# Kernel optimization log

Hardware: AMD Instinct MI355X
Metric: run time of the kernel (lower is better)

The kernel has to match this reference:

```python
import jax, jax.numpy as jnp
import numpy as np

N_NODES = 100000
N_EDGES = 1200000
D = 64


def gcn_conv(x, src, dst, ew, W, b, n):
    # add self-loops with weight 1 (PyG GCNConv default)
    loops = jnp.arange(n)
    s = jnp.concatenate([src, loops])
    d = jnp.concatenate([dst, loops])
    w = jnp.concatenate([ew, jnp.ones((n,), ew.dtype)])
    deg = jax.ops.segment_sum(w, d, num_segments=n)           # [n]
    dis = jnp.where(deg > 0, jax.lax.rsqrt(deg), 0.0)
    norm = dis[s] * w * dis[d]                                # [E+n]
    h = x @ W                                                 # [n, out]
    msg = norm[:, None] * h[s]                                # gather
    out = jax.ops.segment_sum(msg, d, num_segments=n)         # scatter
    return out + b


def setup_inputs() -> dict:
    key = jax.random.key(0)
    ks = jax.random.split(key, 7)
    x = jax.random.normal(ks[0], (N_NODES, D), dtype=jnp.float32)
    edge_index = jax.random.randint(ks[1], (2, N_EDGES), 0, N_NODES, dtype=jnp.int64)
    edge_weight = jax.random.uniform(ks[2], (N_EDGES,), dtype=jnp.float32)
    W1 = jax.random.normal(ks[3], (D, D), dtype=jnp.float32) * (1.0 / np.sqrt(D))
    b1 = jnp.zeros((D,), dtype=jnp.float32)
    W2 = jax.random.normal(ks[4], (D, D), dtype=jnp.float32) * (1.0 / np.sqrt(D))
    b2 = jnp.zeros((D,), dtype=jnp.float32)
    return {"x": x, "edge_index": edge_index, "edge_weight": edge_weight,
            "W1": W1, "b1": b1, "W2": W2, "b2": b2}


def reference(x, edge_index, edge_weight, W1, b1, W2, b2):
    n = x.shape[0]
    src, dst = edge_index[0], edge_index[1]
    x1 = jax.nn.relu(gcn_conv(x, src, dst, edge_weight, W1, b1, n))
    x2 = jax.nn.relu(gcn_conv(x1, src, dst, edge_weight, W2, b2, n))
    return (x1 + x2) * 0.5
```

## Files before the change

### kernel.cpp

```cpp
#include <hip/hip_runtime.h>

#define NN 100000
#define NE 1200000
#define DD 64
#define NBUCK 196
#define BCAP 7168
#define TILE 4096
#define NB1 293
#define NB_G 1563
#define FIX25 33554432.0f
#define FIX25_INV (1.0f/33554432.0f)

typedef short bf16x8 __attribute__((ext_vector_type(8)));
typedef float f32x4  __attribute__((ext_vector_type(4)));

static __device__ __forceinline__ unsigned short f2bf(float f) {
    unsigned int u = __float_as_uint(f);
    unsigned int r = (u + 0x7fffu + ((u >> 16) & 1u)) >> 16;
    return (unsigned short)r;
}
static __device__ __forceinline__ float bf2f(unsigned short s) {
    return __uint_as_float(((unsigned int)s) << 16);
}


__global__ __launch_bounds__(256) void prep(
    int* __restrict__ cursor,
    const float* __restrict__ W1, const float* __restrict__ W2,
    unsigned short* __restrict__ Wt1, unsigned short* __restrict__ Wt2)
{
    if (blockIdx.x == 0) {
        if (threadIdx.x < NBUCK) cursor[threadIdx.x] = 0;
        return;
    }
    const float* W = (blockIdx.x == 1) ? W1 : W2;
    unsigned short* Wt = (blockIdx.x == 1) ? Wt1 : Wt2;
    int t = threadIdx.x;
    int col = t >> 2, k0 = (t & 3) * 16;
    #pragma unroll
    for (int i = 0; i < 16; ++i)
        Wt[col * 64 + k0 + i] = f2bf(W[(k0 + i) * 64 + col]);
}


static __device__ __forceinline__ void gemm_body(
    const float* __restrict__ x, const unsigned short* __restrict__ Wt,
    unsigned short* __restrict__ h16, int r0, int t,
    unsigned short* Xs, unsigned short* Ws)
{
    {
        int col = t >> 2, seg = (t & 3) * 16;
        const uint4* p = (const uint4*)(Wt + col * 64 + seg);
        uint4 a0 = p[0], a1 = p[1];
        *(uint4*)&Ws[col * 72 + seg]     = a0;
        *(uint4*)&Ws[col * 72 + seg + 8] = a1;
    }
    {
        int row = t >> 2, seg = (t & 3) * 16;
        int gr = r0 + row;
        float4 v0 = {0,0,0,0}, v1 = v0, v2 = v0, v3 = v0;
        if (gr < NN) {
            const float4* p = (const float4*)(x + (size_t)gr * DD + seg);
            v0 = p[0]; v1 = p[1]; v2 = p[2]; v3 = p[3];
        }
        ushort4 h0 = { f2bf(v0.x), f2bf(v0.y), f2bf(v0.z), f2bf(v0.w) };
        ushort4 h1 = { f2bf(v1.x), f2bf(v1.y), f2bf(v1.z), f2bf(v1.w) };
        ushort4 h2 = { f2bf(v2.x), f2bf(v2.y), f2bf(v2.z), f2bf(v2.w) };
        ushort4 h3 = { f2bf(v3.x), f2bf(v3.y), f2bf(v3.z), f2bf(v3.w) };
        *(ushort4*)&Xs[row * 72 + seg]      = h0;
        *(ushort4*)&Xs[row * 72 + seg + 4]  = h1;
        *(ushort4*)&Xs[row * 72 + seg + 8]  = h2;
        *(ushort4*)&Xs[row * 72 + seg + 12] = h3;
    }
    __syncthreads();

    const int wv = t >> 6;
    const int ln = t & 63;
    const int m  = ln & 15;
    const int q  = ln >> 4;
    const int arow = wv * 16 + m;

    bf16x8 a0 = *(const bf16x8*)&Xs[arow * 72 + q * 8];
    bf16x8 a1 = *(const bf16x8*)&Xs[arow * 72 + 32 + q * 8];

    f32x4 acc[4];
    #pragma unroll
    for (int c = 0; c < 4; ++c) {
        bf16x8 b0 = *(const bf16x8*)&Ws[(c * 16 + m) * 72 + q * 8];
        bf16x8 b1 = *(const bf16x8*)&Ws[(c * 16 + m) * 72 + 32 + q * 8];
        f32x4 z = {0.f, 0.f, 0.f, 0.f};
        z = __builtin_amdgcn_mfma_f32_16x16x32_bf16(a0, b0, z, 0, 0, 0);
        z = __builtin_amdgcn_mfma_f32_16x16x32_bf16(a1, b1, z, 0, 0, 0);
        acc[c] = z;
    }

    #pragma unroll
    for (int r = 0; r < 4; ++r) {
        int grow = r0 + wv * 16 + q * 4 + r;
        if (grow < NN) {
            #pragma unroll
            for (int c = 0; c < 4; ++c)
                h16[(size_t)grow * DD + c * 16 + m] = f2bf(acc[c][r]);
        }
    }
}


__global__ __launch_bounds__(256) void pass1_gemm(
    const int* __restrict__ src, const int* __restrict__ dst,
    const float* __restrict__ ew, int* __restrict__ cursor,
    unsigned long long* __restrict__ stage,
    const float* __restrict__ x, const unsigned short* __restrict__ Wt1,
    unsigned short* __restrict__ h16)
{
    __shared__ unsigned short Xs[64 * 72];
    __shared__ unsigned short Ws[64 * 72];
    __shared__ int cnt[NBUCK];
    __shared__ int resv[NBUCK];

    const int t = threadIdx.x;

    if (blockIdx.x >= NB1) {
        gemm_body(x, Wt1, h16, (blockIdx.x - NB1) * 64, t, Xs, Ws);
        return;
    }

    const int base = blockIdx.x * TILE;
    if (t < NBUCK) cnt[t] = 0;
    __syncthreads();

    #pragma unroll
    for (int k = 0; k < TILE / 256; ++k) {
        int e = base + k * 256 + t;
        if (e < NE) atomicAdd(&cnt[dst[e] >> 9], 1);
    }
    __syncthreads();
    if (t < NBUCK) {
        int c = cnt[t];
        resv[t] = c ? atomicAdd(&cursor[t], c) : 0;
        cnt[t] = 0;
    }
    __syncthreads();
    #pragma unroll
    for (int k = 0; k < TILE / 256; ++k) {
        int e = base + k * 256 + t;
        if (e < NE) {
            int d = dst[e];
            int b = d >> 9;
            int r = atomicAdd(&cnt[b], 1);
            int pos = resv[b] + r;
            if (pos < BCAP) {
                unsigned int meta = ((unsigned int)(d & 511) << 17) |
                                    (unsigned int)src[e];
                stage[(size_t)b * BCAP + pos] =
                    ((unsigned long long)meta << 32) | __float_as_uint(ew[e]);
            }
        }
    }
}


__global__ __launch_bounds__(512) void pass2(
    const unsigned long long* __restrict__ stage, const int* __restrict__ cursor,
    unsigned int* __restrict__ csr, unsigned int* __restrict__ rowdeg,
    float* __restrict__ dis)
{
    __shared__ unsigned long long sb[BCAP];
    __shared__ int cnt[512];
    __shared__ unsigned sum[512];
    __shared__ int lptr[512];

    const int b = blockIdx.x;
    const int t = threadIdx.x;
    const int n0 = b << 9;
    const int cntb = min(cursor[b], BCAP);

    cnt[t] = 0; sum[t] = 0;
    __syncthreads();

    for (int k = t; k < cntb; k += 512) {
        unsigned long long E = stage[(size_t)b * BCAP + k];
        unsigned int meta = (unsigned int)(E >> 32);
        int dl = meta >> 17;
        float w = __uint_as_float((unsigned int)E);
        int r = atomicAdd(&cnt[dl], 1);
        atomicAdd(&sum[dl], (unsigned)(w * FIX25));
        unsigned int meta2 = ((unsigned int)dl << 23) |
                             ((unsigned int)min(r, 63) << 17) |
                             (meta & 0x1ffffu);
        sb[k] = ((unsigned long long)meta2 << 32) |
                ((r < 64) ? (unsigned long long)f2bf(w) : 0xffffffffull);
    }
    __syncthreads();

    int v = cnt[t];
    __syncthreads();
    for (int off = 1; off < 512; off <<= 1) {
        int add = (t >= off) ? cnt[t - off] : 0;
        __syncthreads();
        cnt[t] += add;
        __syncthreads();
    }
    lptr[t] = cnt[t] - v;

    int node = n0 + t;
    if (node < NN) {
        float deg = 1.0f + (float)sum[t] * FIX25_INV;
        dis[node] = rsqrtf(deg);
        rowdeg[node] = ((unsigned)(b * BCAP + (cnt[t] - v)) << 6) |
                       (unsigned)min(v, 63);
    }
    __syncthreads();

    for (int k = t; k < cntb; k += 512) {
        unsigned long long E = sb[k];
        if ((unsigned int)E == 0xffffffffu) continue;
        unsigned int meta2 = (unsigned int)(E >> 32);
        int dl = meta2 >> 23;
        int r  = (meta2 >> 17) & 63;
        unsigned int s = meta2 & 0x1ffffu;
        csr[b * BCAP + lptr[dl] + r] =
            (s << 15) | ((unsigned int)E & 0x7fffu);
    }
}


__global__ __launch_bounds__(256) void bake(
    unsigned int* __restrict__ csr, const int* __restrict__ cursor,
    const float* __restrict__ dis)
{
    const int b  = blockIdx.x / 7;
    const int k0 = (blockIdx.x % 7) * 1024;
    const int cntb = min(cursor[b], BCAP);
    const int kend = min(k0 + 1024, cntb);
    for (int k = k0 + threadIdx.x; k < kend; k += 256) {
        unsigned int e = csr[b * BCAP + k];
        unsigned int s = e >> 15;
        float nm = dis[s] * bf2f((unsigned short)(e & 0x7fffu));
        csr[b * BCAP + k] = (e & 0xffff8000u) | (f2bf(nm) & 0x7fffu);
    }
}


template <bool FINAL>
__global__ __launch_bounds__(256) void gather(
    const unsigned short* __restrict__ h16, const float* __restrict__ bias,
    const float* __restrict__ dis, const unsigned int* __restrict__ rowdeg,
    const unsigned int* __restrict__ csr,
    const float* __restrict__ prev, float* __restrict__ out)
{
    const int node = __builtin_amdgcn_readfirstlane(
        (blockIdx.x * blockDim.x + threadIdx.x) >> 6);
    const int lane = threadIdx.x & 63;
    if (node >= NN) return;

    const unsigned int rd = rowdeg[node];
    const int deg = rd & 63;
    const float di = dis[node];

    float a0 = fmaf(di * di, bf2f(h16[node * DD + lane]), bias[lane]);
    float a1 = 0.f, a2 = 0.f, a3 = 0.f;

    const unsigned int* seg = csr + (rd >> 6);
    int j = 0;
    for (; j + 3 < deg; j += 4) {
        unsigned int e0 = seg[j],     e1 = seg[j + 1];
        unsigned int e2 = seg[j + 2], e3 = seg[j + 3];
        float n0 = bf2f((unsigned short)(e0 & 0x7fffu)) * di;
        float n1 = bf2f((unsigned short)(e1 & 0x7fffu)) * di;
        float n2 = bf2f((unsigned short)(e2 & 0x7fffu)) * di;
        float n3 = bf2f((unsigned short)(e3 & 0x7fffu)) * di;
        a0 = fmaf(n0, bf2f(h16[(e0 >> 15) * DD + lane]), a0);
        a1 = fmaf(n1, bf2f(h16[(e1 >> 15) * DD + lane]), a1);
        a2 = fmaf(n2, bf2f(h16[(e2 >> 15) * DD + lane]), a2);
        a3 = fmaf(n3, bf2f(h16[(e3 >> 15) * DD + lane]), a3);
    }
    for (; j < deg; ++j) {
        unsigned int e = seg[j];
        a0 = fmaf(bf2f((unsigned short)(e & 0x7fffu)) * di,
                  bf2f(h16[(e >> 15) * DD + lane]), a0);
    }

    float v = fmaxf((a0 + a1) + (a2 + a3), 0.f);
    int idx = node * DD + lane;
    if (FINAL) out[idx] = 0.5f * (prev[idx] + v);
    else       out[idx] = v;
}

__global__ __launch_bounds__(256) void gemm_mfma(
    const float* __restrict__ x, const unsigned short* __restrict__ Wt,
    unsigned short* __restrict__ h16)
{
    __shared__ unsigned short Xs[64 * 72];
    __shared__ unsigned short Ws[64 * 72];
    gemm_body(x, Wt, h16, blockIdx.x * 64, threadIdx.x, Xs, Ws);
}


extern "C" void kernel_launch(void* const* d_in, const int* in_sizes, int n_in,
                              void* d_out, int out_size, void* d_ws, size_t ws_size,
                              hipStream_t stream) {
    const float* x   = (const float*)d_in[0];
    const int*   ei  = (const int*)d_in[1];
    const float* ewt = (const float*)d_in[2];
    const float* W1  = (const float*)d_in[3];
    const float* b1  = (const float*)d_in[4];
    const float* W2  = (const float*)d_in[5];
    const float* b2  = (const float*)d_in[6];
    float* out = (float*)d_out;

    const int* srcv = ei;
    const int* dstv = ei + NE;

    float* wsf = (float*)d_ws;
    int* cursor = (int*)wsf;
    unsigned short* Wt1 = (unsigned short*)(wsf + 256);
    unsigned short* Wt2 = Wt1 + 4096;
    float* dis = wsf + 4352;
    unsigned int* rowdeg = (unsigned int*)(wsf + 104448);
    unsigned long long* stage = (unsigned long long*)(wsf + 204544);
    unsigned int* csr = (unsigned int*)(wsf + 204544 + 2 * NBUCK * BCAP);
    unsigned short* h16 = (unsigned short*)(csr + NBUCK * BCAP);

    const int GB = (NN * 64) / 256;

    prep<<<3, 256, 0, stream>>>(cursor, W1, W2, Wt1, Wt2);
    pass1_gemm<<<NB1 + NB_G, 256, 0, stream>>>(srcv, dstv, ewt, cursor, stage,
                                               x, Wt1, h16);
    pass2<<<NBUCK, 512, 0, stream>>>(stage, cursor, csr, rowdeg, dis);
    bake<<<NBUCK * 7, 256, 0, stream>>>(csr, cursor, dis);

    gather<false><<<GB, 256, 0, stream>>>(h16, b1, dis, rowdeg, csr, nullptr, out);
    gemm_mfma<<<NB_G, 256, 0, stream>>>(out, Wt2, h16);
    gather<true><<<GB, 256, 0, stream>>>(h16, b2, dis, rowdeg, csr, out, out);
}
```

Before: 229.0 us.

## Drop prep and bake kernels, re-read stage in pass2, shuffle edges in gather

The prep kernel is replaced by a memset plus W transposition and bf16 conversion done inside each GEMM block, and the bake kernel is removed. Source normalisation dis[s] is now applied in gather, where each lane loads one CSR entry and the edges are broadcast with wave shuffles. pass2 no longer stages edges in a large LDS buffer and instead re-reads the global stage array in a second pass. The pass1 tile is doubled so fewer blocks do the bucketing. Together these cut kernel launches and LDS use, at the cost of extra global reads in pass2 and a per-edge dis gather in each gather kernel.

```diff
diff --git a/kernel.cpp b/kernel.cpp
--- a/kernel.cpp
+++ b/kernel.cpp
@@ -5,8 +5,8 @@
 #define DD 64
 #define NBUCK 196
 #define BCAP 7168
-#define TILE 4096
-#define NB1 293
+#define TILE 8192
+#define NB1 147
 #define NB_G 1563
 #define FIX25 33554432.0f
 #define FIX25_INV (1.0f/33554432.0f)
@@ -24,36 +24,16 @@
 }
 
 
-__global__ __launch_bounds__(256) void prep(
-    int* __restrict__ cursor,
-    const float* __restrict__ W1, const float* __restrict__ W2,
-    unsigned short* __restrict__ Wt1, unsigned short* __restrict__ Wt2)
-{
-    if (blockIdx.x == 0) {
-        if (threadIdx.x < NBUCK) cursor[threadIdx.x] = 0;
-        return;
-    }
-    const float* W = (blockIdx.x == 1) ? W1 : W2;
-    unsigned short* Wt = (blockIdx.x == 1) ? Wt1 : Wt2;
-    int t = threadIdx.x;
-    int col = t >> 2, k0 = (t & 3) * 16;
-    #pragma unroll
-    for (int i = 0; i < 16; ++i)
-        Wt[col * 64 + k0 + i] = f2bf(W[(k0 + i) * 64 + col]);
-}
-
-
 static __device__ __forceinline__ void gemm_body(
-    const float* __restrict__ x, const unsigned short* __restrict__ Wt,
+    const float* __restrict__ x, const float* __restrict__ W,
     unsigned short* __restrict__ h16, int r0, int t,
     unsigned short* Xs, unsigned short* Ws)
 {
     {
-        int col = t >> 2, seg = (t & 3) * 16;
-        const uint4* p = (const uint4*)(Wt + col * 64 + seg);
-        uint4 a0 = p[0], a1 = p[1];
-        *(uint4*)&Ws[col * 72 + seg]     = a0;
-        *(uint4*)&Ws[col * 72 + seg + 8] = a1;
+        int col = t >> 2, k0 = (t & 3) * 16;
+        #pragma unroll
+        for (int i = 0; i < 16; ++i)
+            Ws[col * 72 + k0 + i] = f2bf(W[(k0 + i) * 64 + col]);
     }
     {
         int row = t >> 2, seg = (t & 3) * 16;
@@ -110,7 +90,7 @@
     const int* __restrict__ src, const int* __restrict__ dst,
     const float* __restrict__ ew, int* __restrict__ cursor,
     unsigned long long* __restrict__ stage,
-    const float* __restrict__ x, const unsigned short* __restrict__ Wt1,
+    const float* __restrict__ x, const float* __restrict__ W1,
     unsigned short* __restrict__ h16)
 {
     __shared__ unsigned short Xs[64 * 72];
@@ -121,7 +101,7 @@
     const int t = threadIdx.x;
 
     if (blockIdx.x >= NB1) {
-        gemm_body(x, Wt1, h16, (blockIdx.x - NB1) * 64, t, Xs, Ws);
+        gemm_body(x, W1, h16, (blockIdx.x - NB1) * 64, t, Xs, Ws);
         return;
     }
 
@@ -129,7 +109,7 @@
     if (t < NBUCK) cnt[t] = 0;
     __syncthreads();
 
-    #pragma unroll
+    #pragma unroll 8
     for (int k = 0; k < TILE / 256; ++k) {
         int e = base + k * 256 + t;
         if (e < NE) atomicAdd(&cnt[dst[e] >> 9], 1);
@@ -141,7 +121,7 @@
         cnt[t] = 0;
     }
     __syncthreads();
-    #pragma unroll
+    #pragma unroll 8
     for (int k = 0; k < TILE / 256; ++k) {
         int e = base + k * 256 + t;
         if (e < NE) {
@@ -165,9 +145,9 @@
     unsigned int* __restrict__ csr, unsigned int* __restrict__ rowdeg,
     float* __restrict__ dis)
 {
-    __shared__ unsigned long long sb[BCAP];
     __shared__ int cnt[512];
     __shared__ unsigned sum[512];
+    __shared__ int scn[512];
     __shared__ int lptr[512];
 
     const int b = blockIdx.x;
@@ -176,6 +156,36 @@
     const int cntb = min(cursor[b], BCAP);
 
     cnt[t] = 0; sum[t] = 0;
+    __syncthreads();
+
+    for (int k = t; k < cntb; k += 512) {
+        unsigned long long E = stage[(size_t)b * BCAP + k];
+        int dl = (int)(E >> 49);
+        float w = __uint_as_float((unsigned int)E);
+        atomicAdd(&cnt[dl], 1);
+        atomicAdd(&sum[dl], (unsigned)(w * FIX25));
+    }
+    __syncthreads();
+
+    int v = cnt[t];
+    scn[t] = v;
+    __syncthreads();
+    for (int off = 1; off < 512; off <<= 1) {
+        int add = (t >= off) ? scn[t - off] : 0;
+        __syncthreads();
+        scn[t] += add;
+        __syncthreads();
+    }
+    lptr[t] = scn[t] - v;
+    cnt[t] = 0;
+
+    int node = n0 + t;
+    if (node < NN) {
+        float deg = 1.0f + (float)sum[t] * FIX25_INV;
+        dis[node] = rsqrtf(deg);
+        rowdeg[node] = ((unsigned)(b * BCAP + lptr[t]) << 6) |
+                       (unsigned)min(v, 63);
+    }
     __syncthreads();
 
     for (int k = t; k < cntb; k += 512) {
@@ -184,60 +194,9 @@
         int dl = meta >> 17;
         float w = __uint_as_float((unsigned int)E);
         int r = atomicAdd(&cnt[dl], 1);
-        atomicAdd(&sum[dl], (unsigned)(w * FIX25));
-        unsigned int meta2 = ((unsigned int)dl << 23) |
-                             ((unsigned int)min(r, 63) << 17) |
-                             (meta & 0x1ffffu);
-        sb[k] = ((unsigned long long)meta2 << 32) |
-                ((r < 64) ? (unsigned long long)f2bf(w) : 0xffffffffull);
-    }
-    __syncthreads();
-
-    int v = cnt[t];
-    __syncthreads();
-    for (int off = 1; off < 512; off <<= 1) {
-        int add = (t >= off) ? cnt[t - off] : 0;
-        __syncthreads();
-        cnt[t] += add;
-        __syncthreads();
-    }
-    lptr[t] = cnt[t] - v;
-
-    int node = n0 + t;
-    if (node < NN) {
-        float deg = 1.0f + (float)sum[t] * FIX25_INV;
-        dis[node] = rsqrtf(deg);
-        rowdeg[node] = ((unsigned)(b * BCAP + (cnt[t] - v)) << 6) |
-                       (unsigned)min(v, 63);
-    }
-    __syncthreads();
-
-    for (int k = t; k < cntb; k += 512) {
-        unsigned long long E = sb[k];
-        if ((unsigned int)E == 0xffffffffu) continue;
-        unsigned int meta2 = (unsigned int)(E >> 32);
-        int dl = meta2 >> 23;
-        int r  = (meta2 >> 17) & 63;
-        unsigned int s = meta2 & 0x1ffffu;
-        csr[b * BCAP + lptr[dl] + r] =
-            (s << 15) | ((unsigned int)E & 0x7fffu);
-    }
-}
-
-
-__global__ __launch_bounds__(256) void bake(
-    unsigned int* __restrict__ csr, const int* __restrict__ cursor,
-    const float* __restrict__ dis)
-{
-    const int b  = blockIdx.x / 7;
-    const int k0 = (blockIdx.x % 7) * 1024;
-    const int cntb = min(cursor[b], BCAP);
-    const int kend = min(k0 + 1024, cntb);
-    for (int k = k0 + threadIdx.x; k < kend; k += 256) {
-        unsigned int e = csr[b * BCAP + k];
-        unsigned int s = e >> 15;
-        float nm = dis[s] * bf2f((unsigned short)(e & 0x7fffu));
-        csr[b * BCAP + k] = (e & 0xffff8000u) | (f2bf(nm) & 0x7fffu);
+        if (r < 63)
+            csr[b * BCAP + lptr[dl] + r] =
+                ((meta & 0x1ffffu) << 15) | (f2bf(w) & 0x7fffu);
     }
 }
 
@@ -258,27 +217,33 @@
     const int deg = rd & 63;
     const float di = dis[node];
 
+    const unsigned int* seg = csr + (rd >> 6);
+    int   s_ln = 0;
+    float n_ln = 0.f;
+    if (lane < deg) {
+        unsigned int e = seg[lane];
+        s_ln = (int)(e >> 15) * DD;
+        n_ln = dis[e >> 15] * bf2f((unsigned short)(e & 0x7fffu)) * di;
+    }
+
     float a0 = fmaf(di * di, bf2f(h16[node * DD + lane]), bias[lane]);
     float a1 = 0.f, a2 = 0.f, a3 = 0.f;
 
-    const unsigned int* seg = csr + (rd >> 6);
     int j = 0;
     for (; j + 3 < deg; j += 4) {
-        unsigned int e0 = seg[j],     e1 = seg[j + 1];
-        unsigned int e2 = seg[j + 2], e3 = seg[j + 3];
-        float n0 = bf2f((unsigned short)(e0 & 0x7fffu)) * di;
-        float n1 = bf2f((unsigned short)(e1 & 0x7fffu)) * di;
-        float n2 = bf2f((unsigned short)(e2 & 0x7fffu)) * di;
-        float n3 = bf2f((unsigned short)(e3 & 0x7fffu)) * di;
-        a0 = fmaf(n0, bf2f(h16[(e0 >> 15) * DD + lane]), a0);
-        a1 = fmaf(n1, bf2f(h16[(e1 >> 15) * DD + lane]), a1);
-        a2 = fmaf(n2, bf2f(h16[(e2 >> 15) * DD + lane]), a2);
-        a3 = fmaf(n3, bf2f(h16[(e3 >> 15) * DD + lane]), a3);
+        int   s0 = __shfl(s_ln, j, 64),     s1 = __shfl(s_ln, j + 1, 64);
+        int   s2 = __shfl(s_ln, j + 2, 64), s3 = __shfl(s_ln, j + 3, 64);
+        float n0 = __shfl(n_ln, j, 64),     n1 = __shfl(n_ln, j + 1, 64);
+        float n2 = __shfl(n_ln, j + 2, 64), n3 = __shfl(n_ln, j + 3, 64);
+        a0 = fmaf(n0, bf2f(h16[s0 + lane]), a0);
+        a1 = fmaf(n1, bf2f(h16[s1 + lane]), a1);
+        a2 = fmaf(n2, bf2f(h16[s2 + lane]), a2);
+        a3 = fmaf(n3, bf2f(h16[s3 + lane]), a3);
     }
     for (; j < deg; ++j) {
-        unsigned int e = seg[j];
-        a0 = fmaf(bf2f((unsigned short)(e & 0x7fffu)) * di,
-                  bf2f(h16[(e >> 15) * DD + lane]), a0);
+        int   s = __shfl(s_ln, j, 64);
+        float n = __shfl(n_ln, j, 64);
+        a0 = fmaf(n, bf2f(h16[s + lane]), a0);
     }
 
     float v = fmaxf((a0 + a1) + (a2 + a3), 0.f);
@@ -288,12 +253,12 @@
 }
 
 __global__ __launch_bounds__(256) void gemm_mfma(
-    const float* __restrict__ x, const unsigned short* __restrict__ Wt,
+    const float* __restrict__ x, const float* __restrict__ W,
     unsigned short* __restrict__ h16)
 {
     __shared__ unsigned short Xs[64 * 72];
     __shared__ unsigned short Ws[64 * 72];
-    gemm_body(x, Wt, h16, blockIdx.x * 64, threadIdx.x, Xs, Ws);
+    gemm_body(x, W, h16, blockIdx.x * 64, threadIdx.x, Xs, Ws);
 }
 
 
@@ -314,23 +279,20 @@
 
     float* wsf = (float*)d_ws;
     int* cursor = (int*)wsf;
-    unsigned short* Wt1 = (unsigned short*)(wsf + 256);
-    unsigned short* Wt2 = Wt1 + 4096;
-    float* dis = wsf + 4352;
-    unsigned int* rowdeg = (unsigned int*)(wsf + 104448);
-    unsigned long long* stage = (unsigned long long*)(wsf + 204544);
-    unsigned int* csr = (unsigned int*)(wsf + 204544 + 2 * NBUCK * BCAP);
+    float* dis = wsf + 256;
+    unsigned int* rowdeg = (unsigned int*)(wsf + 100352);
+    unsigned long long* stage = (unsigned long long*)(wsf + 200448);
+    unsigned int* csr = (unsigned int*)(wsf + 200448 + 2 * NBUCK * BCAP);
     unsigned short* h16 = (unsigned short*)(csr + NBUCK * BCAP);
 
     const int GB = (NN * 64) / 256;
 
-    prep<<<3, 256, 0, stream>>>(cursor, W1, W2, Wt1, Wt2);
+    hipMemsetAsync(cursor, 0, NBUCK * sizeof(int), stream);
     pass1_gemm<<<NB1 + NB_G, 256, 0, stream>>>(srcv, dstv, ewt, cursor, stage,
-                                               x, Wt1, h16);
+                                               x, W1, h16);
     pass2<<<NBUCK, 512, 0, stream>>>(stage, cursor, csr, rowdeg, dis);
-    bake<<<NBUCK * 7, 256, 0, stream>>>(csr, cursor, dis);
 
     gather<false><<<GB, 256, 0, stream>>>(h16, b1, dis, rowdeg, csr, nullptr, out);
-    gemm_mfma<<<NB_G, 256, 0, stream>>>(out, Wt2, h16);
+    gemm_mfma<<<NB_G, 256, 0, stream>>>(out, W2, h16);
     gather<true><<<GB, 256, 0, stream>>>(h16, b2, dis, rowdeg, csr, out, out);
 }
```

New measurement: 248.6 us. 8.6% more time.
